# Optimization experiments

Measured on AMD Instinct MI355X. Metric: run time of the kernel, lower is better.

Reference implementation:

```python
import jax, jax.numpy as jnp
import numpy as np

NUM_NODES = 100000
NUM_EDGES = 625000
IN_FEATURES = 128
OUT_FEATURES = 128


def setup_inputs() -> dict:
    key = jax.random.key(0)
    k1, k2, k3, k4 = jax.random.split(key, 4)
    x = jax.random.normal(k1, (NUM_NODES, IN_FEATURES), dtype=jnp.float32)
    edge_index = jax.random.randint(k2, (2, NUM_EDGES), 0, NUM_NODES, dtype=jnp.int64)
    # Xavier uniform for W (fan_in=IN, fan_out=OUT); B initialized to zeros in the
    # original, but we use small random values so gradients flow through both paths.
    limit = float(np.sqrt(6.0 / (IN_FEATURES + OUT_FEATURES)))
    W = jax.random.uniform(k3, (OUT_FEATURES, IN_FEATURES), dtype=jnp.float32,
                           minval=-limit, maxval=limit)
    B = jax.random.uniform(k4, (OUT_FEATURES, IN_FEATURES), dtype=jnp.float32,
                           minval=-limit, maxval=limit)
    return {"x": x, "edge_index": edge_index, "W": W, "B": B}


def reference(x, edge_index, W, B):
    sources, destinations = edge_index[0], edge_index[1]
    # message: gather destination features, scatter-add into source slots
    messages = x[destinations]                                        # [E, F_in]
    agg = jax.ops.segment_sum(messages, sources, num_segments=x.shape[0])  # [N, F_in]
    # in-degree (w.r.t. sources) normalization; zero-degree -> divide by 1
    deg = jax.ops.segment_sum(jnp.ones((sources.shape[0],), dtype=x.dtype),
                              sources, num_segments=x.shape[0])       # [N]
    deg = jnp.where(deg == 0, jnp.ones_like(deg), deg)
    agg = agg / deg[:, None]
    # update: (W @ messages.T + B @ x.T).T == messages @ W.T + x @ B.T
    out = agg @ W.T + x @ B.T                                         # [N, F_out]
    return out
```

## Files before the change

kernel.cpp:

```cpp
#include <hip/hip_runtime.h>

#define F_IN   128
#define F_OUT  128

typedef __attribute__((ext_vector_type(8))) short short8;
typedef __attribute__((ext_vector_type(4))) float floatx4;

__device__ __forceinline__ float bf16u_to_f_lo(unsigned int u) {
    union { unsigned int i; float f; } c; c.i = u << 16; return c.f;
}
__device__ __forceinline__ float bf16u_to_f_hi(unsigned int u) {
    union { unsigned int i; float f; } c; c.i = u & 0xffff0000u; return c.f;
}
__device__ __forceinline__ unsigned short f_to_bf16(float f) {
    union { float f; unsigned int i; } c; c.f = f;
    unsigned int u = c.i;
    u += 0x7fffu + ((u >> 16) & 1u);
    return (unsigned short)(u >> 16);
}
__device__ __forceinline__ unsigned int pack2(unsigned short a, unsigned short b) {
    return (unsigned int)a | ((unsigned int)b << 16);
}

__device__ __forceinline__ void gload_lds16(const void* g, void* l) {
    __builtin_amdgcn_global_load_lds(
        (const __attribute__((address_space(1))) unsigned int*)g,
        (__attribute__((address_space(3))) unsigned int*)l, 16, 0, 0);
}

__global__ __launch_bounds__(256) void init_kernel(const float* __restrict__ x,
                                                   char* __restrict__ outb,
                                                   const float* __restrict__ W,
                                                   const float* __restrict__ Bm,
                                                   uint4* __restrict__ bfrag,
                                                   int* __restrict__ cnt, int N) {
    long tid = (long)blockIdx.x * blockDim.x + threadIdx.x;
    if (blockIdx.x == gridDim.x - 1) {
        int t = threadIdx.x;
#pragma unroll
        for (int i = 0; i < 16; ++i) {
            int flat = i * 256 + t;
            int lane = flat & 63;
            int idx = flat >> 6;
            int nt = idx >> 3, sfrag = idx & 7;
            int n = nt * 16 + (lane & 15);
            int kbase = sfrag * 32 + (lane >> 4) * 8;
            const float* srcp = (kbase < 128) ? (W + n * 128 + kbase)
                                              : (Bm + n * 128 + (kbase - 128));
            float4 v0 = *(const float4*)srcp;
            float4 v1 = *(const float4*)(srcp + 4);
            uint4 pk;
            pk.x = pack2(f_to_bf16(v0.x), f_to_bf16(v0.y));
            pk.y = pack2(f_to_bf16(v0.z), f_to_bf16(v0.w));
            pk.z = pack2(f_to_bf16(v1.x), f_to_bf16(v1.y));
            pk.w = pack2(f_to_bf16(v1.z), f_to_bf16(v1.w));
            bfrag[flat] = pk;
        }
        return;
    }
    if (tid < N) cnt[tid] = 0;
    if (tid < (long)N * 32) {
        int row = (int)(tid >> 5);
        int seg = (int)(tid & 31);
        float4 v = *(const float4*)(x + (size_t)row * 128 + seg * 4);
        unsigned short r[4] = {f_to_bf16(v.x), f_to_bf16(v.y), f_to_bf16(v.z), f_to_bf16(v.w)};
        *(ushort4*)(outb + (size_t)row * 512 + 256 + seg * 8) =
            make_ushort4(r[0], r[1], r[2], r[3]);
    }
}

__global__ void hist_kernel(const int* __restrict__ src, int* __restrict__ cnt, int E) {
    int e = blockIdx.x * blockDim.x + threadIdx.x;
    if (e < E) atomicAdd(&cnt[src[e]], 1);
}

__global__ __launch_bounds__(256) void scan_kernel(const int* __restrict__ cnt,
                                                   int* __restrict__ off, int n) {
    __shared__ int s[256];
    __shared__ int red[256];
    int b = blockIdx.x, t = threadIdx.x;
    long pre = (long)b * 1024;
    int sum = 0;
    for (long i = (long)t * 4; i < pre; i += 1024) {
        int4 v = *(const int4*)&cnt[i];
        sum += v.x + v.y + v.z + v.w;
    }
    red[t] = sum;
    __syncthreads();
    for (int d = 128; d > 0; d >>= 1) {
        if (t < d) red[t] += red[t + d];
        __syncthreads();
    }
    int base = red[0];
    int cbase = b * 1024 + t * 4;
    int v[4];
#pragma unroll
    for (int j = 0; j < 4; ++j) {
        int i = cbase + j;
        v[j] = (i < n) ? cnt[i] : 0;
    }
    int l1 = v[0], l2 = l1 + v[1], l3 = l2 + v[2], tot = l3 + v[3];
    s[t] = tot;
    __syncthreads();
    for (int d = 1; d < 256; d <<= 1) {
        int val = s[t];
        int add = (t >= d) ? s[t - d] : 0;
        __syncthreads();
        s[t] = val + add;
        __syncthreads();
    }
    int thr_excl = ((t > 0) ? s[t - 1] : 0) + base;
    if (cbase + 0 < n) off[cbase + 0] = thr_excl;
    if (cbase + 1 < n) off[cbase + 1] = thr_excl + l1;
    if (cbase + 2 < n) off[cbase + 2] = thr_excl + l2;
    if (cbase + 3 < n) off[cbase + 3] = thr_excl + l3;
}

__global__ void fill_kernel(const int* __restrict__ ei, int* __restrict__ off,
                            int* __restrict__ dst_sorted, int E) {
    int e = blockIdx.x * blockDim.x + threadIdx.x;
    if (e < E) {
        int s = ei[e];
        int d = ei[E + e];
        int p = atomicAdd(&off[s], 1);
        dst_sorted[p] = d;
    }
}

__global__ __launch_bounds__(256) void gather_bf16_kernel(const int* __restrict__ off,
                                                          const int* __restrict__ dst_sorted,
                                                          char* __restrict__ outb, int N) {
    int node = blockIdx.x * 16 + (threadIdx.x >> 4);
    int lane = threadIdx.x & 15;
    if (node >= N) return;
    int start = (node == 0) ? 0 : off[node - 1];
    int end = off[node];
    float acc[8];
#pragma unroll
    for (int i = 0; i < 8; ++i) acc[i] = 0.0f;

    const char* xb = outb;
    int j = start;
    for (; j + 4 <= end; j += 4) {
        int d0 = dst_sorted[j];
        int d1 = dst_sorted[j + 1];
        int d2 = dst_sorted[j + 2];
        int d3 = dst_sorted[j + 3];
        uint4 a = *(const uint4*)(xb + (size_t)d0 * 512 + 256 + lane * 16);
        uint4 b = *(const uint4*)(xb + (size_t)d1 * 512 + 256 + lane * 16);
        uint4 c = *(const uint4*)(xb + (size_t)d2 * 512 + 256 + lane * 16);
        uint4 d = *(const uint4*)(xb + (size_t)d3 * 512 + 256 + lane * 16);
        acc[0] += bf16u_to_f_lo(a.x); acc[1] += bf16u_to_f_hi(a.x);
        acc[2] += bf16u_to_f_lo(a.y); acc[3] += bf16u_to_f_hi(a.y);
        acc[4] += bf16u_to_f_lo(a.z); acc[5] += bf16u_to_f_hi(a.z);
        acc[6] += bf16u_to_f_lo(a.w); acc[7] += bf16u_to_f_hi(a.w);
        acc[0] += bf16u_to_f_lo(b.x); acc[1] += bf16u_to_f_hi(b.x);
        acc[2] += bf16u_to_f_lo(b.y); acc[3] += bf16u_to_f_hi(b.y);
        acc[4] += bf16u_to_f_lo(b.z); acc[5] += bf16u_to_f_hi(b.z);
        acc[6] += bf16u_to_f_lo(b.w); acc[7] += bf16u_to_f_hi(b.w);
        acc[0] += bf16u_to_f_lo(c.x); acc[1] += bf16u_to_f_hi(c.x);
        acc[2] += bf16u_to_f_lo(c.y); acc[3] += bf16u_to_f_hi(c.y);
        acc[4] += bf16u_to_f_lo(c.z); acc[5] += bf16u_to_f_hi(c.z);
        acc[6] += bf16u_to_f_lo(c.w); acc[7] += bf16u_to_f_hi(c.w);
        acc[0] += bf16u_to_f_lo(d.x); acc[1] += bf16u_to_f_hi(d.x);
        acc[2] += bf16u_to_f_lo(d.y); acc[3] += bf16u_to_f_hi(d.y);
        acc[4] += bf16u_to_f_lo(d.z); acc[5] += bf16u_to_f_hi(d.z);
        acc[6] += bf16u_to_f_lo(d.w); acc[7] += bf16u_to_f_hi(d.w);
    }
    for (; j < end; ++j) {
        int d0 = dst_sorted[j];
        uint4 a = *(const uint4*)(xb + (size_t)d0 * 512 + 256 + lane * 16);
        acc[0] += bf16u_to_f_lo(a.x); acc[1] += bf16u_to_f_hi(a.x);
        acc[2] += bf16u_to_f_lo(a.y); acc[3] += bf16u_to_f_hi(a.y);
        acc[4] += bf16u_to_f_lo(a.z); acc[5] += bf16u_to_f_hi(a.z);
        acc[6] += bf16u_to_f_lo(a.w); acc[7] += bf16u_to_f_hi(a.w);
    }
    int deg = end - start;
    float scale = (deg > 0) ? (1.0f / (float)deg) : 1.0f;
    unsigned short r[8];
#pragma unroll
    for (int i = 0; i < 8; ++i) r[i] = f_to_bf16(acc[i] * scale);
    uint4 pk;
    pk.x = pack2(r[0], r[1]);
    pk.y = pack2(r[2], r[3]);
    pk.z = pack2(r[4], r[5]);
    pk.w = pack2(r[6], r[7]);
    *(uint4*)(outb + (size_t)node * 512 + lane * 16) = pk;
}

__global__ __launch_bounds__(256, 2) void gemm_mfma_kernel(const uint4* __restrict__ bfrag,
                                                           float* __restrict__ out, int N) {
    __shared__ uint4 Bs[4096];
    int t = threadIdx.x;
    int lane = t & 63;
    int w = t >> 6;
    int m16 = lane & 15;
    int quad = lane >> 4;

#pragma unroll
    for (int j = 0; j < 16; ++j)
        gload_lds16(bfrag + (w * 16 + j) * 64 + lane, &Bs[(w * 16 + j) * 64]);

    int rowbase = blockIdx.x * 128 + w * 32;
    short8 afrag[2][8];
#pragma unroll
    for (int g = 0; g < 2; ++g) {
        int arow = rowbase + g * 16 + m16;
        if (arow > N - 1) arow = N - 1;
        const char* ab = (const char*)out + (size_t)arow * 512;
#pragma unroll
        for (int s = 0; s < 8; ++s)
            afrag[g][s] = *(const short8*)(ab + s * 64 + quad * 16);
    }
    __syncthreads();

    floatx4 acc[2][8];
#pragma unroll
    for (int g = 0; g < 2; ++g)
#pragma unroll
        for (int nt = 0; nt < 8; ++nt) acc[g][nt] = (floatx4){0.f, 0.f, 0.f, 0.f};

#pragma unroll
    for (int nt = 0; nt < 8; ++nt) {
#pragma unroll
        for (int s = 0; s < 8; ++s) {
            short8 bf = *(const short8*)&Bs[(nt * 8 + s) * 64 + lane];
            acc[0][nt] = __builtin_amdgcn_mfma_f32_16x16x32_bf16(afrag[0][s], bf, acc[0][nt], 0, 0, 0);
            acc[1][nt] = __builtin_amdgcn_mfma_f32_16x16x32_bf16(afrag[1][s], bf, acc[1][nt], 0, 0, 0);
        }
    }

#pragma unroll
    for (int g = 0; g < 2; ++g)
#pragma unroll
        for (int nt = 0; nt < 8; ++nt)
#pragma unroll
            for (int r = 0; r < 4; ++r) {
                int gr = rowbase + g * 16 + quad * 4 + r;
                if (gr < N) out[(size_t)gr * 128 + nt * 16 + m16] = acc[g][nt][r];
            }
}

__global__ void zero_kernel(int* __restrict__ p, long n) {
    long i = (long)blockIdx.x * blockDim.x + threadIdx.x;
    long stride = (long)gridDim.x * blockDim.x;
    for (; i < n; i += stride) p[i] = 0;
}

__global__ void invdeg_kernel(int* __restrict__ deg_io, int N) {
    int i = blockIdx.x * blockDim.x + threadIdx.x;
    if (i < N) {
        int d = deg_io[i];
        float inv = (d > 0) ? (1.0f / (float)d) : 1.0f;
        ((float*)deg_io)[i] = inv;
    }
}

__global__ __launch_bounds__(128) void scatter_atomic_kernel(const float* __restrict__ x,
                                                             const int* __restrict__ ei,
                                                             const float* __restrict__ invdeg,
                                                             float* __restrict__ out, int E) {
    int e = blockIdx.x;
    int f = threadIdx.x;
    int s = ei[e];
    int d = ei[E + e];
    float v = x[(long)d * F_IN + f] * invdeg[s];
    atomicAdd(&out[(long)s * F_IN + f], v);
}

__global__ __launch_bounds__(256) void gemm_fused_kernel(const float* __restrict__ x,
                                                         const float* __restrict__ W,
                                                         const float* __restrict__ Bm,
                                                         float* __restrict__ out, int N) {
    __shared__ float As[64][68];
    __shared__ float Ms[64][132];
    int t = threadIdx.x;
    int row0 = blockIdx.x * 64;
    int c0 = (t & 31) * 4;
    int r0 = (t >> 5) * 8;
    float acc[8][4];
#pragma unroll
    for (int i = 0; i < 8; ++i)
#pragma unroll
        for (int j = 0; j < 4; ++j) acc[i][j] = 0.0f;

    for (int kc = 0; kc < 4; ++kc) {
        const float* Asrc = (kc < 2) ? out : x;
        const float* Msrc = (kc < 2) ? W : Bm;
        int k0 = (kc & 1) * 64;
#pragma unroll
        for (int i = 0; i < 4; ++i) {
            int flat = t + 256 * i;
            int m = flat >> 4, ks = flat & 15;
            int row = row0 + m;
            float4 v = make_float4(0.f, 0.f, 0.f, 0.f);
            if (row < N) v = *(const float4*)&Asrc[(long)row * 128 + k0 + ks * 4];
            As[ks * 4 + 0][m] = v.x;
            As[ks * 4 + 1][m] = v.y;
            As[ks * 4 + 2][m] = v.z;
            As[ks * 4 + 3][m] = v.w;
        }
#pragma unroll
        for (int i = 0; i < 8; ++i) {
            int flat = t + 256 * i;
            int c = flat >> 4, ks = flat & 15;
            float4 v = *(const float4*)&Msrc[(long)c * 128 + k0 + ks * 4];
            Ms[ks * 4 + 0][c] = v.x;
            Ms[ks * 4 + 1][c] = v.y;
            Ms[ks * 4 + 2][c] = v.z;
            Ms[ks * 4 + 3][c] = v.w;
        }
        __syncthreads();
#pragma unroll 8
        for (int kk = 0; kk < 64; ++kk) {
            float4 a0 = *(const float4*)&As[kk][r0];
            float4 a1 = *(const float4*)&As[kk][r0 + 4];
            float4 m0 = *(const float4*)&Ms[kk][c0];
            float a[8] = {a0.x, a0.y, a0.z, a0.w, a1.x, a1.y, a1.z, a1.w};
            float m[4] = {m0.x, m0.y, m0.z, m0.w};
#pragma unroll
            for (int i = 0; i < 8; ++i)
#pragma unroll
                for (int j = 0; j < 4; ++j) acc[i][j] += a[i] * m[j];
        }
        __syncthreads();
    }
#pragma unroll
    for (int i = 0; i < 8; ++i) {
        int row = row0 + r0 + i;
        if (row < N) {
            float4 v = make_float4(acc[i][0], acc[i][1], acc[i][2], acc[i][3]);
            *(float4*)&out[(long)row * 128 + c0] = v;
        }
    }
}


extern "C" void kernel_launch(void* const* d_in, const int* in_sizes, int n_in,
                              void* d_out, int out_size, void* d_ws, size_t ws_size,
                              hipStream_t stream) {
    const float* x = (const float*)d_in[0];
    const int* ei = (const int*)d_in[1];
    const float* W = (const float*)d_in[2];
    const float* Bm = (const float*)d_in[3];
    float* out = (float*)d_out;

    const int N = in_sizes[0] / F_IN;
    const int E = in_sizes[1] / 2;
    const int NCHUNK = (N + 1023) / 1024;

    const size_t need_main = 4096 * sizeof(uint4) + ((size_t)2 * N + (size_t)E) * sizeof(int);
    const size_t need_deg  = (size_t)N * sizeof(int);

    if (ws_size >= need_main) {
        uint4* bfrag      = (uint4*)d_ws;
        int*   cnt        = (int*)(bfrag + 4096);
        int*   off        = cnt + N;
        int*   dst_sorted = off + N;

        {
            long tot = (long)N * 32;
            int nb = (int)((tot + 255) / 256) + 1;
            init_kernel<<<nb, 256, 0, stream>>>(x, (char*)out, W, Bm, bfrag, cnt, N);
        }
        hist_kernel<<<(E + 255) / 256, 256, 0, stream>>>(ei, cnt, E);
        scan_kernel<<<NCHUNK, 256, 0, stream>>>(cnt, off, N);
        fill_kernel<<<(E + 255) / 256, 256, 0, stream>>>(ei, off, dst_sorted, E);
        gather_bf16_kernel<<<(N + 15) / 16, 256, 0, stream>>>(off, dst_sorted, (char*)out, N);
        gemm_mfma_kernel<<<(N + 127) / 128, 256, 0, stream>>>(bfrag, out, N);
    } else if (ws_size >= need_deg) {
        int* deg = (int*)d_ws;
        zero_kernel<<<256, 256, 0, stream>>>(deg, N);
        hist_kernel<<<(E + 255) / 256, 256, 0, stream>>>(ei, deg, E);
        invdeg_kernel<<<(N + 255) / 256, 256, 0, stream>>>(deg, N);
        zero_kernel<<<512, 256, 0, stream>>>((int*)out, (long)N * F_IN);
        scatter_atomic_kernel<<<E, 128, 0, stream>>>(x, ei, (const float*)deg, out, E);
        gemm_fused_kernel<<<(N + 63) / 64, 256, 0, stream>>>(x, W, Bm, out, N);
    }
}
```

Baseline: 234.6 us.

## Fuse scan and CSR fill into per-bucket kernel with LDS staging

Replaces the separate prefix-scan and global-atomic fill kernels with one kernel in which each block owns a contiguous range of 392 source nodes. The block computes its global offset base, scans its local counts in shared memory, then streams the entire source-index array and keeps only edges that fall in its range. It places those edges with shared-memory atomics into an LDS staging buffer and writes them out contiguously. This removes one launch, the scattered global atomics and the random destination writes. In exchange, every block rereads the whole edge list, and the kernel relies on L2 bandwidth to absorb that redundant traffic.

```diff
diff --git a/kernel.cpp b/kernel.cpp
--- a/kernel.cpp
+++ b/kernel.cpp
@@ -2,6 +2,8 @@
 
 #define F_IN   128
 #define F_OUT  128
+#define B0     392
+#define FCAP   4096
 
 typedef __attribute__((ext_vector_type(8))) short short8;
 typedef __attribute__((ext_vector_type(4))) float floatx4;
@@ -74,14 +76,21 @@
     if (e < E) atomicAdd(&cnt[src[e]], 1);
 }
 
-__global__ __launch_bounds__(256) void scan_kernel(const int* __restrict__ cnt,
-                                                   int* __restrict__ off, int n) {
-    __shared__ int s[256];
+__global__ __launch_bounds__(256) void bucketfill_kernel(const int* __restrict__ ei,
+                                                         const int* __restrict__ cnt,
+                                                         int* __restrict__ off,
+                                                         int* __restrict__ dst_sorted,
+                                                         int N, int E) {
     __shared__ int red[256];
+    __shared__ int sc[512];
+    __shared__ int cur[512];
+    __shared__ int stage[FCAP];
     int b = blockIdx.x, t = threadIdx.x;
-    long pre = (long)b * 1024;
+    int lo = b * B0;
+    int hi = min(N, lo + B0);
+
     int sum = 0;
-    for (long i = (long)t * 4; i < pre; i += 1024) {
+    for (int i = t * 4; i + 3 < lo; i += 1024) {
         int4 v = *(const int4*)&cnt[i];
         sum += v.x + v.y + v.z + v.w;
     }
@@ -92,39 +101,61 @@
         __syncthreads();
     }
     int base = red[0];
-    int cbase = b * 1024 + t * 4;
-    int v[4];
-#pragma unroll
-    for (int j = 0; j < 4; ++j) {
-        int i = cbase + j;
-        v[j] = (i < n) ? cnt[i] : 0;
-    }
-    int l1 = v[0], l2 = l1 + v[1], l3 = l2 + v[2], tot = l3 + v[3];
-    s[t] = tot;
-    __syncthreads();
-    for (int d = 1; d < 256; d <<= 1) {
-        int val = s[t];
-        int add = (t >= d) ? s[t - d] : 0;
+    __syncthreads();
+
+    sc[t] = (lo + t < hi) ? cnt[lo + t] : 0;
+    sc[t + 256] = (lo + t + 256 < hi) ? cnt[lo + t + 256] : 0;
+    __syncthreads();
+    for (int d = 1; d < 512; d <<= 1) {
+        int v0 = sc[t] + ((t >= d) ? sc[t - d] : 0);
+        int i1 = t + 256;
+        int v1 = sc[i1] + ((i1 >= d) ? sc[i1 - d] : 0);
         __syncthreads();
-        s[t] = val + add;
+        sc[t] = v0; sc[i1] = v1;
         __syncthreads();
     }
-    int thr_excl = ((t > 0) ? s[t - 1] : 0) + base;
-    if (cbase + 0 < n) off[cbase + 0] = thr_excl;
-    if (cbase + 1 < n) off[cbase + 1] = thr_excl + l1;
-    if (cbase + 2 < n) off[cbase + 2] = thr_excl + l2;
-    if (cbase + 3 < n) off[cbase + 3] = thr_excl + l3;
-}
-
-__global__ void fill_kernel(const int* __restrict__ ei, int* __restrict__ off,
-                            int* __restrict__ dst_sorted, int E) {
-    int e = blockIdx.x * blockDim.x + threadIdx.x;
-    if (e < E) {
-        int s = ei[e];
-        int d = ei[E + e];
-        int p = atomicAdd(&off[s], 1);
-        dst_sorted[p] = d;
-    }
+    int total = sc[511];
+    if (lo + t < hi) {
+        off[lo + t] = base + sc[t];
+        cur[t] = (t > 0) ? sc[t - 1] : 0;
+    }
+    {
+        int i1 = t + 256;
+        if (lo + i1 < hi) {
+            off[lo + i1] = base + sc[i1];
+            cur[i1] = sc[i1 - 1];
+        }
+    }
+    __syncthreads();
+
+    const int E4 = E & ~3;
+    for (int idx = t * 4; idx < E4; idx += 1024) {
+        int4 s4 = *(const int4*)&ei[idx];
+        int ss[4] = {s4.x, s4.y, s4.z, s4.w};
+#pragma unroll
+        for (int j = 0; j < 4; ++j) {
+            int s = ss[j];
+            if (s >= lo && s < hi) {
+                int rel = atomicAdd(&cur[s - lo], 1);
+                int d = ei[E + idx + j];
+                if (rel < FCAP) stage[rel] = d;
+                else dst_sorted[base + rel] = d;
+            }
+        }
+    }
+    for (int idx = E4 + t; idx < E; idx += 256) {
+        int s = ei[idx];
+        if (s >= lo && s < hi) {
+            int rel = atomicAdd(&cur[s - lo], 1);
+            int d = ei[E + idx];
+            if (rel < FCAP) stage[rel] = d;
+            else dst_sorted[base + rel] = d;
+        }
+    }
+    __syncthreads();
+
+    int tc = min(total, FCAP);
+    for (int r = t; r < tc; r += 256) dst_sorted[base + r] = stage[r];
 }
 
 __global__ __launch_bounds__(256) void gather_bf16_kernel(const int* __restrict__ off,
@@ -347,7 +378,6 @@
 
     const int N = in_sizes[0] / F_IN;
     const int E = in_sizes[1] / 2;
-    const int NCHUNK = (N + 1023) / 1024;
 
     const size_t need_main = 4096 * sizeof(uint4) + ((size_t)2 * N + (size_t)E) * sizeof(int);
     const size_t need_deg  = (size_t)N * sizeof(int);
@@ -364,8 +394,7 @@
             init_kernel<<<nb, 256, 0, stream>>>(x, (char*)out, W, Bm, bfrag, cnt, N);
         }
         hist_kernel<<<(E + 255) / 256, 256, 0, stream>>>(ei, cnt, E);
-        scan_kernel<<<NCHUNK, 256, 0, stream>>>(cnt, off, N);
-        fill_kernel<<<(E + 255) / 256, 256, 0, stream>>>(ei, off, dst_sorted, E);
+        bucketfill_kernel<<<(N + B0 - 1) / B0, 256, 0, stream>>>(ei, cnt, off, dst_sorted, N, E);
         gather_bf16_kernel<<<(N + 15) / 16, 256, 0, stream>>>(off, dst_sorted, (char*)out, N);
         gemm_mfma_kernel<<<(N + 127) / 128, 256, 0, stream>>>(bfrag, out, N);
     } else if (ws_size >= need_deg) {
```

New measurement: 433.5 us. +84.7%, slower.
